# Performance work log

Measured on AMD Instinct MI355X. Metric: run time of the kernel, lower is better.

## Reference

```python
import jax, jax.numpy as jnp
import numpy as np

N = 100000  # nodes
E = 1600000  # edges
F = 128      # features
C = 16       # classes
K = 2        # propagation hops


def setup_inputs() -> dict:
    key = jax.random.key(0)
    k1, k2, k3 = jax.random.split(key, 3)
    x = jax.random.normal(k1, (N, F), dtype=jnp.float32)
    edge_index = jax.random.randint(k2, (2, E), 0, N, dtype=jnp.int64)
    W = jax.random.normal(k3, (F, C), dtype=jnp.float32) * (1.0 / np.sqrt(F))
    b = jnp.zeros((C,), dtype=jnp.float32)
    return {"x": x, "edge_index": edge_index, "W": W, "b": b}


def _sg_propagate(x, row, col, num_nodes):
    # GCN symmetric normalization with self-loops already appended to row/col.
    ones = jnp.ones(row.shape, dtype=x.dtype)
    deg = jax.ops.segment_sum(ones, row, num_segments=num_nodes)
    dinv = jnp.where(deg > 0, jax.lax.rsqrt(deg), jnp.zeros_like(deg))
    norm = dinv[row] * dinv[col]  # [E+N]
    for _ in range(K):
        # gather messages from source nodes, scale, scatter-sum to destinations
        x = jax.ops.segment_sum(norm[:, None] * x[col], row, num_segments=num_nodes)
    return x


def reference(x, edge_index, W, b):
    num_nodes = x.shape[0]
    loops = jnp.arange(num_nodes, dtype=edge_index.dtype)
    row = jnp.concatenate([edge_index[0], loops])
    col = jnp.concatenate([edge_index[1], loops])
    h = _sg_propagate(x, row, col, num_nodes)  # [N, F]
    logits = h @ W + b                          # [N, C]
    return jax.nn.log_softmax(logits, axis=1)
```

## Files before the change

### kernel.cpp

```cpp
#include <hip/hip_runtime.h>
#include <hip/hip_fp16.h>
#include <math.h>

#define NN 100000
#define NE 1600000
#define NF 128
#define NC 16
#define NBUK 391
#define BSH 8
#define BNODES 256
#define CHUNK 4096
#define P1B 391
#define CMASK 0x1FFFF
#define MAXEDG 4800

__global__ void k_init(int* __restrict__ bcur) {
    int n = threadIdx.x;
    if (n < NBUK) bcur[n] = n * MAXEDG;
}

__global__ __launch_bounds__(256) void k_part(const int* __restrict__ row,
                                              const int* __restrict__ col,
                                              int* __restrict__ bcur,
                                              int* __restrict__ pairs) {
    __shared__ int hist[NBUK];
    __shared__ int loff[NBUK];
    __shared__ int gbase[NBUK];
    __shared__ int stage[CHUNK];
    __shared__ unsigned short bkt[CHUNK];
    const int t = threadIdx.x;
    const int cb = blockIdx.x * CHUNK;
    const int ccnt = min(CHUNK, NE - cb);
    const int nquad = ccnt >> 2;
    for (int i = t; i < NBUK; i += 256) hist[i] = 0;
    __syncthreads();

    int rr[16], cc[16], rk[16];
    #pragma unroll
    for (int j = 0; j < 4; ++j) {
        int q = j * 256 + t;
        if (q < nquad) {
            int4 r4 = *(const int4*)&row[cb + 4 * q];
            int4 c4 = *(const int4*)&col[cb + 4 * q];
            rr[4 * j] = r4.x; rr[4 * j + 1] = r4.y; rr[4 * j + 2] = r4.z; rr[4 * j + 3] = r4.w;
            cc[4 * j] = c4.x; cc[4 * j + 1] = c4.y; cc[4 * j + 2] = c4.z; cc[4 * j + 3] = c4.w;
            #pragma unroll
            for (int k = 0; k < 4; ++k)
                rk[4 * j + k] = atomicAdd(&hist[rr[4 * j + k] >> BSH], 1);
        }
    }
    __syncthreads();
    if (t < 64) {
        int loc[7];
        int acc = 0;
        #pragma unroll
        for (int j = 0; j < 7; ++j) {
            int idx = t * 7 + j;
            int v = (idx < NBUK) ? hist[idx] : 0;
            loc[j] = acc;
            acc += v;
        }
        int s = acc;
        #pragma unroll
        for (int o = 1; o < 64; o <<= 1) {
            int u = __shfl_up(s, o, 64);
            if (t >= o) s += u;
        }
        int excl = s - acc;
        #pragma unroll
        for (int j = 0; j < 7; ++j) {
            int idx = t * 7 + j;
            if (idx < NBUK) loff[idx] = excl + loc[j];
        }
    }
    __syncthreads();
    for (int i = t; i < NBUK; i += 256)
        if (hist[i] > 0) gbase[i] = atomicAdd(&bcur[i], hist[i]);
    __syncthreads();
    #pragma unroll
    for (int j = 0; j < 4; ++j) {
        int q = j * 256 + t;
        if (q < nquad) {
            #pragma unroll
            for (int k = 0; k < 4; ++k) {
                int r = rr[4 * j + k];
                int b = r >> BSH;
                int pos = loff[b] + rk[4 * j + k];
                stage[pos] = ((r & (BNODES - 1)) << 17) | cc[4 * j + k];
                bkt[pos] = (unsigned short)b;
            }
        }
    }
    __syncthreads();
    for (int s = t; s < ccnt; s += 256) {
        int b = bkt[s];
        pairs[gbase[b] + (s - loff[b])] = stage[s];
    }
}

__global__ __launch_bounds__(256) void k_fine(const int* __restrict__ bcur,
                                              const int* __restrict__ pairs,
                                              int2* __restrict__ rpc,
                                              float* __restrict__ dinv,
                                              int* __restrict__ csr) {
    __shared__ int h[BNODES];
    __shared__ int hs[BNODES];
    const int b = blockIdx.x;
    const int nb = b << BSH;
    const int t = threadIdx.x;
    h[t] = 0;
    __syncthreads();
    const int st = b * MAXEDG;
    const int m = bcur[b] - st;
    for (int i = t; i < m; i += 256)
        atomicAdd(&h[__builtin_nontemporal_load(&pairs[st + i]) >> 17], 1);
    __syncthreads();
    int v = h[t];
    hs[t] = v;
    __syncthreads();
    for (int o = 1; o < 256; o <<= 1) {
        int a = (t >= o) ? hs[t - o] : 0;
        __syncthreads();
        hs[t] += a;
        __syncthreads();
    }
    int excl = hs[t] - v;
    int n0 = nb + t;
    if (n0 < NN) {
        rpc[n0] = make_int2(st + excl, v);
        dinv[n0] = rsqrtf((float)(v + 1));
    }
    __syncthreads();
    h[t] = excl;
    __syncthreads();
    for (int i = t; i < m; i += 256) {
        int pk = __builtin_nontemporal_load(&pairs[st + i]);
        int pos = atomicAdd(&h[pk >> 17], 1);
        csr[st + pos] = pk & CMASK;
    }
}

#define GEMM_ROWS 64
#define XPAD (NF + 4)

__global__ __launch_bounds__(256) void k_gemm(const float* __restrict__ x,
                                              const float* __restrict__ W,
                                              const float* __restrict__ dinv,
                                              __half* __restrict__ u) {
    __shared__ float Wl[NF * NC];
    __shared__ float xs[GEMM_ROWS * XPAD];
    const int t = threadIdx.x;
    for (int i = t; i < NF * NC; i += 256) Wl[i] = W[i];
    const int rbase = blockIdx.x * GEMM_ROWS;
    const float4* x4 = (const float4*)x;
    for (int i = t; i < GEMM_ROWS * (NF / 4); i += 256) {
        int lrow = i / (NF / 4), k4 = i - lrow * (NF / 4);
        int r = rbase + lrow;
        float4 v = (r < NN) ? x4[(size_t)r * (NF / 4) + k4]
                            : make_float4(0.f, 0.f, 0.f, 0.f);
        *(float4*)&xs[lrow * XPAD + 4 * k4] = v;
    }
    __syncthreads();
    const int lr = t >> 2;
    const int cg = t & 3;
    float4 acc = make_float4(0.f, 0.f, 0.f, 0.f);
    #pragma unroll
    for (int k = 0; k < NF; ++k) {
        float xv = xs[lr * XPAD + k];
        float4 w = *(const float4*)&Wl[k * NC + cg * 4];
        acc.x = fmaf(xv, w.x, acc.x);
        acc.y = fmaf(xv, w.y, acc.y);
        acc.z = fmaf(xv, w.z, acc.z);
        acc.w = fmaf(xv, w.w, acc.w);
    }
    int r = rbase + lr;
    if (r < NN) {
        float d = dinv[r];
        __half2 h0 = __floats2half2_rn(acc.x * d, acc.y * d);
        __half2 h1 = __floats2half2_rn(acc.z * d, acc.w * d);
        float2 o;
        o.x = *(float*)&h0;
        o.y = *(float*)&h1;
        ((float2*)u)[((size_t)r << 2) + cg] = o;
    }
}


__device__ __forceinline__ void acc8(float2 rw, float& a0, float& a1,
                                     float& a2, float& a3) {
    __half2 p0 = *(__half2*)&rw.x;
    __half2 p1 = *(__half2*)&rw.y;
    float2 f0 = __half22float2(p0);
    float2 f1 = __half22float2(p1);
    a0 += f0.x; a1 += f0.y; a2 += f1.x; a3 += f1.y;
}

__global__ __launch_bounds__(256) void k_hop1(const int2* __restrict__ rpc,
                                              const float* __restrict__ dinv,
                                              const int* __restrict__ csr,
                                              const float2* __restrict__ u,
                                              float2* __restrict__ u1) {
    int t = blockIdx.x * 256 + threadIdx.x;
    if (t >= NN * 4) return;
    int n = t >> 2, c4 = t & 3;
    int2 rc = rpc[n];
    int s = rc.x, m = rc.y;
    float a0 = 0.f, a1 = 0.f, a2 = 0.f, a3 = 0.f;
    acc8(u[(n << 2) + c4], a0, a1, a2, a3);
    int i = 0;
    for (; i + 8 <= m; i += 8) {
        int cc[8];
        #pragma unroll
        for (int j = 0; j < 8; ++j) cc[j] = __builtin_nontemporal_load(&csr[s + i + j]);
        #pragma unroll
        for (int j = 0; j < 8; ++j) acc8(u[(cc[j] << 2) + c4], a0, a1, a2, a3);
    }
    for (; i < m; ++i)
        acc8(u[(__builtin_nontemporal_load(&csr[s + i]) << 2) + c4], a0, a1, a2, a3);
    float d = dinv[n];
    float sc = d * d;
    __half2 h0 = __floats2half2_rn(a0 * sc, a1 * sc);
    __half2 h1 = __floats2half2_rn(a2 * sc, a3 * sc);
    float2 o;
    o.x = *(float*)&h0;
    o.y = *(float*)&h1;
    u1[t] = o;
}

__global__ __launch_bounds__(256) void k_hop2(const int2* __restrict__ rpc,
                                              const float* __restrict__ dinv,
                                              const int* __restrict__ csr,
                                              const float2* __restrict__ u1,
                                              const float* __restrict__ bias,
                                              float* __restrict__ out) {
    int t = blockIdx.x * 256 + threadIdx.x;
    if (t >= NN * 4) return;
    int n = t >> 2, c4 = t & 3;
    int2 rc = rpc[n];
    int s = rc.x, m = rc.y;
    float a0 = 0.f, a1 = 0.f, a2 = 0.f, a3 = 0.f;
    acc8(u1[(n << 2) + c4], a0, a1, a2, a3);
    int i = 0;
    for (; i + 8 <= m; i += 8) {
        int cc[8];
        #pragma unroll
        for (int j = 0; j < 8; ++j) cc[j] = __builtin_nontemporal_load(&csr[s + i + j]);
        #pragma unroll
        for (int j = 0; j < 8; ++j) acc8(u1[(cc[j] << 2) + c4], a0, a1, a2, a3);
    }
    for (; i < m; ++i)
        acc8(u1[(__builtin_nontemporal_load(&csr[s + i]) << 2) + c4], a0, a1, a2, a3);
    float d = dinv[n];
    float4 bv = ((const float4*)bias)[c4];
    float v0 = fmaf(d, a0, bv.x);
    float v1 = fmaf(d, a1, bv.y);
    float v2 = fmaf(d, a2, bv.z);
    float v3 = fmaf(d, a3, bv.w);
    float mx = fmaxf(fmaxf(v0, v1), fmaxf(v2, v3));
    #pragma unroll
    for (int o = 2; o > 0; o >>= 1) mx = fmaxf(mx, __shfl_xor(mx, o, 4));
    float sm = expf(v0 - mx) + expf(v1 - mx) + expf(v2 - mx) + expf(v3 - mx);
    #pragma unroll
    for (int o = 2; o > 0; o >>= 1) sm += __shfl_xor(sm, o, 4);
    float lse = mx + logf(sm);
    float4 o;
    o.x = v0 - lse; o.y = v1 - lse; o.z = v2 - lse; o.w = v3 - lse;
    ((float4*)out)[t] = o;
}

extern "C" void kernel_launch(void* const* d_in, const int* in_sizes, int n_in,
                              void* d_out, int out_size, void* d_ws, size_t ws_size,
                              hipStream_t stream) {
    const float* x    = (const float*)d_in[0];
    const int*   ei   = (const int*)d_in[1];
    const float* W    = (const float*)d_in[2];
    const float* bias = (const float*)d_in[3];
    float* out = (float*)d_out;

    const int* row = ei;
    const int* col = ei + NE;

    char* ws = (char*)d_ws;
    size_t off = 0;
    auto carve = [&](size_t bytes) -> void* {
        void* p = ws + off;
        off += (bytes + 255) & ~(size_t)255;
        return p;
    };
    int2*   rpc   = (int2*)  carve((size_t)NN * sizeof(int2));
    float*  dinv  = (float*) carve((size_t)NN * sizeof(float));
    int*    bcur  = (int*)   carve((size_t)NBUK * sizeof(int));
    int*    pairs = (int*)   carve((size_t)NBUK * MAXEDG * sizeof(int));
    int*    csr   = (int*)   carve((size_t)NBUK * MAXEDG * sizeof(int));
    float2* u     = (float2*)carve((size_t)NN * NC * sizeof(__half));
    float2* u1    = (float2*)carve((size_t)NN * NC * sizeof(__half));

    k_init<<<1, 512, 0, stream>>>(bcur);
    k_part<<<P1B, 256, 0, stream>>>(row, col, bcur, pairs);
    k_fine<<<NBUK, 256, 0, stream>>>(bcur, pairs, rpc, dinv, csr);

    k_gemm<<<(NN + GEMM_ROWS - 1) / GEMM_ROWS, 256, 0, stream>>>(x, W, dinv, (__half*)u);

    const int HB = (NN * 4 + 255) / 256;
    k_hop1<<<HB, 256, 0, stream>>>(rpc, dinv, csr, u, u1);
    k_hop2<<<HB, 256, 0, stream>>>(rpc, dinv, csr, u1, bias, out);
}
```

Before: 105.6 us.

## Widen hop gathers to 16-byte loads, vectorize GEMM LDS, enlarge partition chunks

```diff
diff --git a/kernel.cpp b/kernel.cpp
--- a/kernel.cpp
+++ b/kernel.cpp
@@ -9,8 +9,8 @@
 #define NBUK 391
 #define BSH 8
 #define BNODES 256
-#define CHUNK 4096
-#define P1B 391
+#define CHUNK 8192
+#define P1B 196
 #define CMASK 0x1FFFF
 #define MAXEDG 4800
 
@@ -19,7 +19,7 @@
     if (n < NBUK) bcur[n] = n * MAXEDG;
 }
 
-__global__ __launch_bounds__(256) void k_part(const int* __restrict__ row,
+__global__ __launch_bounds__(512) void k_part(const int* __restrict__ row,
                                               const int* __restrict__ col,
                                               int* __restrict__ bcur,
                                               int* __restrict__ pairs) {
@@ -32,13 +32,13 @@
     const int cb = blockIdx.x * CHUNK;
     const int ccnt = min(CHUNK, NE - cb);
     const int nquad = ccnt >> 2;
-    for (int i = t; i < NBUK; i += 256) hist[i] = 0;
+    for (int i = t; i < NBUK; i += 512) hist[i] = 0;
     __syncthreads();
 
     int rr[16], cc[16], rk[16];
     #pragma unroll
     for (int j = 0; j < 4; ++j) {
-        int q = j * 256 + t;
+        int q = j * 512 + t;
         if (q < nquad) {
             int4 r4 = *(const int4*)&row[cb + 4 * q];
             int4 c4 = *(const int4*)&col[cb + 4 * q];
@@ -74,12 +74,12 @@
         }
     }
     __syncthreads();
-    for (int i = t; i < NBUK; i += 256)
+    for (int i = t; i < NBUK; i += 512)
         if (hist[i] > 0) gbase[i] = atomicAdd(&bcur[i], hist[i]);
     __syncthreads();
     #pragma unroll
     for (int j = 0; j < 4; ++j) {
-        int q = j * 256 + t;
+        int q = j * 512 + t;
         if (q < nquad) {
             #pragma unroll
             for (int k = 0; k < 4; ++k) {
@@ -92,7 +92,7 @@
         }
     }
     __syncthreads();
-    for (int s = t; s < ccnt; s += 256) {
+    for (int s = t; s < ccnt; s += 512) {
         int b = bkt[s];
         pairs[gbase[b] + (s - loff[b])] = stage[s];
     }
@@ -154,7 +154,7 @@
     const int rbase = blockIdx.x * GEMM_ROWS;
     const float4* x4 = (const float4*)x;
     for (int i = t; i < GEMM_ROWS * (NF / 4); i += 256) {
-        int lrow = i / (NF / 4), k4 = i - lrow * (NF / 4);
+        int lrow = i >> 5, k4 = i & 31;
         int r = rbase + lrow;
         float4 v = (r < NN) ? x4[(size_t)r * (NF / 4) + k4]
                             : make_float4(0.f, 0.f, 0.f, 0.f);
@@ -165,13 +165,16 @@
     const int cg = t & 3;
     float4 acc = make_float4(0.f, 0.f, 0.f, 0.f);
     #pragma unroll
-    for (int k = 0; k < NF; ++k) {
-        float xv = xs[lr * XPAD + k];
-        float4 w = *(const float4*)&Wl[k * NC + cg * 4];
-        acc.x = fmaf(xv, w.x, acc.x);
-        acc.y = fmaf(xv, w.y, acc.y);
-        acc.z = fmaf(xv, w.z, acc.z);
-        acc.w = fmaf(xv, w.w, acc.w);
+    for (int k4 = 0; k4 < NF / 4; ++k4) {
+        float4 xv = *(const float4*)&xs[lr * XPAD + 4 * k4];
+        float4 w0 = *(const float4*)&Wl[(4 * k4 + 0) * NC + cg * 4];
+        float4 w1 = *(const float4*)&Wl[(4 * k4 + 1) * NC + cg * 4];
+        float4 w2 = *(const float4*)&Wl[(4 * k4 + 2) * NC + cg * 4];
+        float4 w3 = *(const float4*)&Wl[(4 * k4 + 3) * NC + cg * 4];
+        acc.x = fmaf(xv.x, w0.x, fmaf(xv.y, w1.x, fmaf(xv.z, w2.x, fmaf(xv.w, w3.x, acc.x))));
+        acc.y = fmaf(xv.x, w0.y, fmaf(xv.y, w1.y, fmaf(xv.z, w2.y, fmaf(xv.w, w3.y, acc.y))));
+        acc.z = fmaf(xv.x, w0.z, fmaf(xv.y, w1.z, fmaf(xv.z, w2.z, fmaf(xv.w, w3.z, acc.z))));
+        acc.w = fmaf(xv.x, w0.w, fmaf(xv.y, w1.w, fmaf(xv.z, w2.w, fmaf(xv.w, w3.w, acc.w))));
     }
     int r = rbase + lr;
     if (r < NN) {
@@ -186,86 +189,95 @@
 }
 
 
-__device__ __forceinline__ void acc8(float2 rw, float& a0, float& a1,
-                                     float& a2, float& a3) {
-    __half2 p0 = *(__half2*)&rw.x;
-    __half2 p1 = *(__half2*)&rw.y;
-    float2 f0 = __half22float2(p0);
-    float2 f1 = __half22float2(p1);
-    a0 += f0.x; a1 += f0.y; a2 += f1.x; a3 += f1.y;
+__device__ __forceinline__ void acc16(float4 rw, float* a) {
+    float2 f0 = __half22float2(*(__half2*)&rw.x);
+    float2 f1 = __half22float2(*(__half2*)&rw.y);
+    float2 f2 = __half22float2(*(__half2*)&rw.z);
+    float2 f3 = __half22float2(*(__half2*)&rw.w);
+    a[0] += f0.x; a[1] += f0.y; a[2] += f1.x; a[3] += f1.y;
+    a[4] += f2.x; a[5] += f2.y; a[6] += f3.x; a[7] += f3.y;
 }
 
 __global__ __launch_bounds__(256) void k_hop1(const int2* __restrict__ rpc,
                                               const float* __restrict__ dinv,
                                               const int* __restrict__ csr,
-                                              const float2* __restrict__ u,
-                                              float2* __restrict__ u1) {
+                                              const float4* __restrict__ u,
+                                              float4* __restrict__ u1) {
     int t = blockIdx.x * 256 + threadIdx.x;
-    if (t >= NN * 4) return;
-    int n = t >> 2, c4 = t & 3;
+    if (t >= NN * 2) return;
+    int n = t >> 1, half = t & 1;
     int2 rc = rpc[n];
     int s = rc.x, m = rc.y;
-    float a0 = 0.f, a1 = 0.f, a2 = 0.f, a3 = 0.f;
-    acc8(u[(n << 2) + c4], a0, a1, a2, a3);
+    float a[8] = {0.f, 0.f, 0.f, 0.f, 0.f, 0.f, 0.f, 0.f};
+    acc16(u[(n << 1) + half], a);
     int i = 0;
     for (; i + 8 <= m; i += 8) {
         int cc[8];
         #pragma unroll
         for (int j = 0; j < 8; ++j) cc[j] = __builtin_nontemporal_load(&csr[s + i + j]);
         #pragma unroll
-        for (int j = 0; j < 8; ++j) acc8(u[(cc[j] << 2) + c4], a0, a1, a2, a3);
+        for (int j = 0; j < 8; ++j) acc16(u[(cc[j] << 1) + half], a);
     }
     for (; i < m; ++i)
-        acc8(u[(__builtin_nontemporal_load(&csr[s + i]) << 2) + c4], a0, a1, a2, a3);
+        acc16(u[(__builtin_nontemporal_load(&csr[s + i]) << 1) + half], a);
     float d = dinv[n];
     float sc = d * d;
-    __half2 h0 = __floats2half2_rn(a0 * sc, a1 * sc);
-    __half2 h1 = __floats2half2_rn(a2 * sc, a3 * sc);
-    float2 o;
-    o.x = *(float*)&h0;
-    o.y = *(float*)&h1;
+    __half2 h0 = __floats2half2_rn(a[0] * sc, a[1] * sc);
+    __half2 h1 = __floats2half2_rn(a[2] * sc, a[3] * sc);
+    __half2 h2 = __floats2half2_rn(a[4] * sc, a[5] * sc);
+    __half2 h3 = __floats2half2_rn(a[6] * sc, a[7] * sc);
+    float4 o;
+    o.x = *(float*)&h0; o.y = *(float*)&h1;
+    o.z = *(float*)&h2; o.w = *(float*)&h3;
     u1[t] = o;
 }
 
 __global__ __launch_bounds__(256) void k_hop2(const int2* __restrict__ rpc,
                                               const float* __restrict__ dinv,
                                               const int* __restrict__ csr,
-                                              const float2* __restrict__ u1,
+                                              const float4* __restrict__ u1,
                                               const float* __restrict__ bias,
                                               float* __restrict__ out) {
     int t = blockIdx.x * 256 + threadIdx.x;
-    if (t >= NN * 4) return;
-    int n = t >> 2, c4 = t & 3;
+    if (t >= NN * 2) return;
+    int n = t >> 1, half = t & 1;
     int2 rc = rpc[n];
     int s = rc.x, m = rc.y;
-    float a0 = 0.f, a1 = 0.f, a2 = 0.f, a3 = 0.f;
-    acc8(u1[(n << 2) + c4], a0, a1, a2, a3);
+    float a[8] = {0.f, 0.f, 0.f, 0.f, 0.f, 0.f, 0.f, 0.f};
+    acc16(u1[(n << 1) + half], a);
     int i = 0;
     for (; i + 8 <= m; i += 8) {
         int cc[8];
         #pragma unroll
         for (int j = 0; j < 8; ++j) cc[j] = __builtin_nontemporal_load(&csr[s + i + j]);
         #pragma unroll
-        for (int j = 0; j < 8; ++j) acc8(u1[(cc[j] << 2) + c4], a0, a1, a2, a3);
+        for (int j = 0; j < 8; ++j) acc16(u1[(cc[j] << 1) + half], a);
     }
     for (; i < m; ++i)
-        acc8(u1[(__builtin_nontemporal_load(&csr[s + i]) << 2) + c4], a0, a1, a2, a3);
+        acc16(u1[(__builtin_nontemporal_load(&csr[s + i]) << 1) + half], a);
     float d = dinv[n];
-    float4 bv = ((const float4*)bias)[c4];
-    float v0 = fmaf(d, a0, bv.x);
-    float v1 = fmaf(d, a1, bv.y);
-    float v2 = fmaf(d, a2, bv.z);
-    float v3 = fmaf(d, a3, bv.w);
-    float mx = fmaxf(fmaxf(v0, v1), fmaxf(v2, v3));
-    #pragma unroll
-    for (int o = 2; o > 0; o >>= 1) mx = fmaxf(mx, __shfl_xor(mx, o, 4));
-    float sm = expf(v0 - mx) + expf(v1 - mx) + expf(v2 - mx) + expf(v3 - mx);
-    #pragma unroll
-    for (int o = 2; o > 0; o >>= 1) sm += __shfl_xor(sm, o, 4);
+    float v[8];
+    const float4* b4 = (const float4*)bias;
+    float4 bv0 = b4[half * 2], bv1 = b4[half * 2 + 1];
+    v[0] = fmaf(d, a[0], bv0.x); v[1] = fmaf(d, a[1], bv0.y);
+    v[2] = fmaf(d, a[2], bv0.z); v[3] = fmaf(d, a[3], bv0.w);
+    v[4] = fmaf(d, a[4], bv1.x); v[5] = fmaf(d, a[5], bv1.y);
+    v[6] = fmaf(d, a[6], bv1.z); v[7] = fmaf(d, a[7], bv1.w);
+    float mx = v[0];
+    #pragma unroll
+    for (int j = 1; j < 8; ++j) mx = fmaxf(mx, v[j]);
+    mx = fmaxf(mx, __shfl_xor(mx, 1, 2));
+    float sm = 0.f;
+    #pragma unroll
+    for (int j = 0; j < 8; ++j) sm += expf(v[j] - mx);
+    sm += __shfl_xor(sm, 1, 2);
     float lse = mx + logf(sm);
-    float4 o;
-    o.x = v0 - lse; o.y = v1 - lse; o.z = v2 - lse; o.w = v3 - lse;
-    ((float4*)out)[t] = o;
+    float4* o4 = (float4*)out;
+    float4 o0, o1;
+    o0.x = v[0] - lse; o0.y = v[1] - lse; o0.z = v[2] - lse; o0.w = v[3] - lse;
+    o1.x = v[4] - lse; o1.y = v[5] - lse; o1.z = v[6] - lse; o1.w = v[7] - lse;
+    o4[((size_t)n << 2) + half * 2]     = o0;
+    o4[((size_t)n << 2) + half * 2 + 1] = o1;
 }
 
 extern "C" void kernel_launch(void* const* d_in, const int* in_sizes, int n_in,
@@ -292,16 +304,16 @@
     int*    bcur  = (int*)   carve((size_t)NBUK * sizeof(int));
     int*    pairs = (int*)   carve((size_t)NBUK * MAXEDG * sizeof(int));
     int*    csr   = (int*)   carve((size_t)NBUK * MAXEDG * sizeof(int));
-    float2* u     = (float2*)carve((size_t)NN * NC * sizeof(__half));
-    float2* u1    = (float2*)carve((size_t)NN * NC * sizeof(__half));
+    float4* u     = (float4*)carve((size_t)NN * NC * sizeof(__half));
+    float4* u1    = (float4*)carve((size_t)NN * NC * sizeof(__half));
 
     k_init<<<1, 512, 0, stream>>>(bcur);
-    k_part<<<P1B, 256, 0, stream>>>(row, col, bcur, pairs);
+    k_part<<<P1B, 512, 0, stream>>>(row, col, bcur, pairs);
     k_fine<<<NBUK, 256, 0, stream>>>(bcur, pairs, rpc, dinv, csr);
 
     k_gemm<<<(NN + GEMM_ROWS - 1) / GEMM_ROWS, 256, 0, stream>>>(x, W, dinv, (__half*)u);
 
-    const int HB = (NN * 4 + 255) / 256;
+    const int HB = (NN * 2 + 255) / 256;
     k_hop1<<<HB, 256, 0, stream>>>(rpc, dinv, csr, u, u1);
     k_hop2<<<HB, 256, 0, stream>>>(rpc, dinv, csr, u1, bias, out);
 }
```

New measurement: 101.5 us. 3.9% less time.
